# Kernel tuning notes

Measured on AMD Instinct MI355X. Metric: run time of the kernel, lower is better.

## Reference

```python
import jax, jax.numpy as jnp
import numpy as np

B, N = 4, 8192


def _nn_idx(a, b):
    # For each point in a [B,Na,3], index of nearest point in b [B,Nb,3].
    # ||a-b||^2 = ||a||^2 - 2 a.b + ||b||^2 ; ||a||^2 is constant per row -> drop it.
    d = jnp.sum(b * b, axis=-1)[:, None, :] - 2.0 * jnp.einsum('bnd,bmd->bnm', a, b)
    return jnp.argmin(d, axis=-1)  # [B, Na]


def _thickness(white, pial):
    # Mirrors compute_thickness_vector: white = inner, pial = outer.
    bix = jnp.arange(white.shape[0])[:, None]
    i1 = _nn_idx(white, pial)            # NN in pial for each white point
    inner_th = pial[bix, i1] - white     # [B, Nw, 3]
    i2 = _nn_idx(pial, white)            # NN in white for each pial point
    outer_th = pial - white[bix, i2]     # [B, Np, 3]
    return inner_th, outer_th


def _msn(a, b):
    # MeanSquaredNormLoss with w=None: mean over all points of sum((a-b)^2, -1)
    return jnp.mean(jnp.sum((a - b) ** 2, axis=-1))


def _sym(a, b, i_a, i_b):
    # SymmetricMeanSquaredNormLoss.forward (batch_size > 1 path, no weights)
    bix = jnp.arange(a.shape[0])[:, None]
    return 0.5 * (_msn(a, b[bix, i_a]) + _msn(a[bix, i_b], b))


def setup_inputs() -> dict:
    key = jax.random.key(0)
    ks = jax.random.split(key, 8)
    return {
        'pred_white': jax.random.normal(ks[0], (B, N, 3), jnp.float32),
        'pred_pial': jax.random.normal(ks[1], (B, N, 3), jnp.float32),
        'true_white': jax.random.normal(ks[2], (B, N, 3), jnp.float32),
        'true_pial': jax.random.normal(ks[3], (B, N, 3), jnp.float32),
        'i_pred_white': jax.random.randint(ks[4], (B, N), 0, N, jnp.int32),
        'i_true_white': jax.random.randint(ks[5], (B, N), 0, N, jnp.int32),
        'i_pred_pial': jax.random.randint(ks[6], (B, N), 0, N, jnp.int32),
        'i_true_pial': jax.random.randint(ks[7], (B, N), 0, N, jnp.int32),
    }


def reference(pred_white, pred_pial, true_white, true_pial,
              i_pred_white, i_true_white, i_pred_pial, i_true_pial):
    yp_inner, yp_outer = _thickness(pred_white, pred_pial)
    yt_inner, yt_outer = _thickness(true_white, true_pial)
    return (0.5 * _sym(yp_inner, yt_inner, i_pred_white, i_true_white)
            + 0.5 * _sym(yp_outer, yt_outer, i_pred_pial, i_true_pial))
```

## Files before the change

kernel.cpp:

```cpp
#include <hip/hip_runtime.h>
#include <math.h>

#define BATCH 4
#define NPTS 8192
#define BN (BATCH * NPTS)
#define NZB 16
#define QK 8
#define QBLK (256 * QK)
#define SUBT 64


__device__ __forceinline__ void pick_ab(int z, const float* pw, const float* pp,
                                        const float* tw, const float* tp,
                                        const float** qa, const float** cb) {
  if (z == 0)      { *qa = pw; *cb = pp; }
  else if (z == 1) { *qa = pp; *cb = pw; }
  else if (z == 2) { *qa = tw; *cb = tp; }
  else             { *qa = tp; *cb = tw; }
}

template <int SPL>
__global__ __launch_bounds__(256, 4) void nn_partial_kernel(
    const float* __restrict__ pw, const float* __restrict__ pp,
    const float* __restrict__ tw, const float* __restrict__ tp,
    float* __restrict__ part_d, unsigned char* __restrict__ part_t) {
  constexpr int SLICE = NPTS / SPL;
  constexpr int NSUB = SLICE / SUBT;
  __shared__ float4 sh[SLICE];

  const int zb = blockIdx.z;
  const int z = zb >> 2;
  const int b = zb & 3;
  const float* qa;
  const float* cb;
  pick_ab(z, pw, pp, tw, tp, &qa, &cb);

  const int tid = threadIdx.x;
  const int cslice = blockIdx.y * SLICE;
  const float* cbb = cb + (size_t)b * NPTS * 3;

  for (int m = tid; m < SLICE; m += 256) {
    const float* c = cbb + (size_t)(cslice + m) * 3;
    const float bx = c[0], by = c[1], bz = c[2];
    sh[m] = make_float4(bx, by, bz, fmaf(bx, bx, fmaf(by, by, bz * bz)));
  }
  __syncthreads();

  const int qbase = blockIdx.x * QBLK;
  float qx[QK], qy[QK], qz[QK], dmin[QK];
  int tile[QK];
  #pragma unroll
  for (int k = 0; k < QK; ++k) {
    const int n = qbase + tid + k * 256;
    const float* q = qa + ((size_t)b * NPTS + n) * 3;
    qx[k] = -2.0f * q[0];
    qy[k] = -2.0f * q[1];
    qz[k] = -2.0f * q[2];
    dmin[k] = INFINITY;
    tile[k] = 0;
  }

  for (int sub = 0; sub < NSUB; ++sub) {
    float pre[QK];
    #pragma unroll
    for (int k = 0; k < QK; ++k) pre[k] = dmin[k];

    const int cb0 = sub * SUBT;
    #pragma unroll 2
    for (int p = 0; p < SUBT / 2; ++p) {
      const float4 c0 = sh[cb0 + 2 * p];
      const float4 c1 = sh[cb0 + 2 * p + 1];
      float t0[QK], t1[QK];
      #pragma unroll
      for (int k = 0; k < QK; ++k)
        t0[k] = fmaf(qx[k], c0.x, fmaf(qy[k], c0.y, fmaf(qz[k], c0.z, c0.w)));
      #pragma unroll
      for (int k = 0; k < QK; ++k)
        t1[k] = fmaf(qx[k], c1.x, fmaf(qy[k], c1.y, fmaf(qz[k], c1.z, c1.w)));
      #pragma unroll
      for (int k = 0; k < QK; ++k)
        dmin[k] = fminf(fminf(t0[k], t1[k]), dmin[k]);
    }
    const int g = blockIdx.y * NSUB + sub;
    #pragma unroll
    for (int k = 0; k < QK; ++k)
      tile[k] = (dmin[k] < pre[k]) ? g : tile[k];
  }

  #pragma unroll
  for (int k = 0; k < QK; ++k) {
    const int n = qbase + tid + k * 256;
    const size_t o = (size_t)blockIdx.y * (NZB * NPTS) + (size_t)zb * NPTS + n;
    part_d[o] = dmin[k];
    part_t[o] = (unsigned char)tile[k];
  }
}

template <int SPL>
__global__ __launch_bounds__(1024) void nn_merge_rescan_kernel(
    const float* __restrict__ pw, const float* __restrict__ pp,
    const float* __restrict__ tw, const float* __restrict__ tp,
    const float* __restrict__ part_d, const unsigned char* __restrict__ part_t,
    int* __restrict__ idx_all, double* __restrict__ acc,
    unsigned int* __restrict__ ticket) {
  __shared__ float md[16][64];
  __shared__ int mg[16][64];
  __shared__ float sdq[64];
  __shared__ int sgq[64];

  if (blockIdx.x == 0 && threadIdx.x == 0) { *acc = 0.0; *ticket = 0u; }

  const int tid = threadIdx.x;
  const int wv = tid >> 6;
  const int lane = tid & 63;
  const int qid0 = blockIdx.x * 64;

  {
    float bd = INFINITY;
    int bg = 0x7fffffff;
    for (int s = wv; s < SPL; s += 16) {
      const size_t o = (size_t)s * (NZB * NPTS) + qid0 + lane;
      const float d = part_d[o];
      const int g = part_t[o];
      if (d < bd || (d == bd && g < bg)) { bd = d; bg = g; }
    }
    md[wv][lane] = bd;
    mg[wv][lane] = bg;
  }
  __syncthreads();
  if (wv == 0) {
    float bd = md[0][lane];
    int bg = mg[0][lane];
    #pragma unroll
    for (int v = 1; v < 16; ++v) {
      const float d = md[v][lane];
      const int g = mg[v][lane];
      if (d < bd || (d == bd && g < bg)) { bd = d; bg = g; }
    }
    sdq[lane] = bd;
    sgq[lane] = bg;
  }
  __syncthreads();

  const int zb = qid0 >> 13;
  const int z = zb >> 2;
  const int b = zb & 3;
  const float* qa;
  const float* cb;
  pick_ab(z, pw, pp, tw, tp, &qa, &cb);
  const float* qb0 = qa + (size_t)b * NPTS * 3;
  const float* cbb = cb + (size_t)b * NPTS * 3;
  const int n0 = qid0 & (NPTS - 1);

  #pragma unroll
  for (int j = 0; j < 4; ++j) {
    const int lq = wv * 4 + j;
    const float best_d = sdq[lq];
    const int best_g = sgq[lq];
    const float* q = qb0 + (size_t)(n0 + lq) * 3;
    const float qx = -2.0f * q[0];
    const float qy = -2.0f * q[1];
    const float qz = -2.0f * q[2];
    const int m = best_g * SUBT + lane;
    const float* c = cbb + (size_t)m * 3;
    const float bx = c[0], by = c[1], bz = c[2];
    const float b2 = fmaf(bx, bx, fmaf(by, by, bz * bz));
    const float dd = fmaf(qx, bx, fmaf(qy, by, fmaf(qz, bz, b2)));
    const unsigned long long hit = __ballot(dd == best_d);
    if (lane == 0)
      idx_all[qid0 + lq] = best_g * SUBT + (__ffsll((long long)hit) - 1);
  }
}

__device__ __forceinline__ float3 ld3(const float* __restrict__ p, int i) {
  const float* q = p + (size_t)i * 3;
  return make_float3(q[0], q[1], q[2]);
}

__device__ __forceinline__ float diff_nrm2(float3 a1, float3 a2, float3 b1, float3 b2) {
  const float x = (a1.x - a2.x) - (b1.x - b2.x);
  const float y = (a1.y - a2.y) - (b1.y - b2.y);
  const float z = (a1.z - a2.z) - (b1.z - b2.z);
  return fmaf(x, x, fmaf(y, y, z * z));
}

__global__ __launch_bounds__(256) void loss_final_kernel(
    const float* __restrict__ pw, const float* __restrict__ pp,
    const float* __restrict__ tw, const float* __restrict__ tp,
    const int* __restrict__ ipw, const int* __restrict__ itw,
    const int* __restrict__ ipp, const int* __restrict__ itp,
    const int* __restrict__ idx_all, double* __restrict__ acc,
    unsigned int* __restrict__ ticket, float* __restrict__ out) {
  __shared__ double sd[4];

  const int gid = blockIdx.x * 256 + threadIdx.x;
  const int term = blockIdx.y;
  const int b = gid >> 13;
  const int n = gid & (NPTS - 1);
  const int base = b * NPTS;

  const float* PW = pw + (size_t)base * 3;
  const float* PP = pp + (size_t)base * 3;
  const float* TW = tw + (size_t)base * 3;
  const float* TP = tp + (size_t)base * 3;
  const int* I1P = idx_all + (0 * BATCH + b) * NPTS;
  const int* I2P = idx_all + (1 * BATCH + b) * NPTS;
  const int* I1T = idx_all + (2 * BATCH + b) * NPTS;
  const int* I2T = idx_all + (3 * BATCH + b) * NPTS;

  float sv;
  if (term == 0) {
    const int j = ipw[base + n];
    sv = diff_nrm2(ld3(PP, I1P[n]), ld3(PW, n), ld3(TP, I1T[j]), ld3(TW, j));
  } else if (term == 1) {
    const int k = itw[base + n];
    sv = diff_nrm2(ld3(PP, I1P[k]), ld3(PW, k), ld3(TP, I1T[n]), ld3(TW, n));
  } else if (term == 2) {
    const int j = ipp[base + n];
    sv = diff_nrm2(ld3(PP, n), ld3(PW, I2P[n]), ld3(TP, j), ld3(TW, I2T[j]));
  } else {
    const int k = itp[base + n];
    sv = diff_nrm2(ld3(PP, k), ld3(PW, I2P[k]), ld3(TP, n), ld3(TW, I2T[n]));
  }

  double ds = (double)sv;
  #pragma unroll
  for (int o = 32; o > 0; o >>= 1) ds += __shfl_down(ds, o, 64);
  if ((threadIdx.x & 63) == 0) sd[threadIdx.x >> 6] = ds;
  __syncthreads();

  if (threadIdx.x == 0) {
    const double bsum = sd[0] + sd[1] + sd[2] + sd[3];
    const double old = atomicAdd(acc, bsum);
    const unsigned int inc = 1u + (unsigned int)(((unsigned long long)
                             __double_as_longlong(old)) & 0ull);
    const unsigned int total = gridDim.x * gridDim.y;
    const unsigned int t = atomicAdd(ticket, inc);
    if (t == total - 1u) {
      const double fin = atomicAdd(acc, 0.0);
      out[0] = (float)(0.25 * fin / (double)BN);
    }
  }
}

template <int SPL>
static void run_pipeline(const float* pw, const float* pp, const float* tw,
                         const float* tp, const int* ipw, const int* itw,
                         const int* ipp, const int* itp, char* ws, float* out,
                         hipStream_t stream) {
  double* acc = (double*)ws;
  unsigned int* ticket = (unsigned int*)(ws + 8);
  int* idx_all = (int*)(ws + 64);
  float* part_d = (float*)(ws + 64 + (size_t)NZB * NPTS * 4);
  unsigned char* part_t =
      (unsigned char*)(ws + 64 + (size_t)NZB * NPTS * 4 +
                       (size_t)SPL * NZB * NPTS * 4);

  dim3 grid_nn(NPTS / QBLK, SPL, NZB);
  nn_partial_kernel<SPL><<<grid_nn, 256, 0, stream>>>(pw, pp, tw, tp, part_d,
                                                      part_t);
  nn_merge_rescan_kernel<SPL><<<(NZB * NPTS) / 64, 1024, 0, stream>>>(
      pw, pp, tw, tp, part_d, part_t, idx_all, acc, ticket);

  dim3 grid_loss(BN / 256, 4);
  loss_final_kernel<<<grid_loss, 256, 0, stream>>>(
      pw, pp, tw, tp, ipw, itw, ipp, itp, idx_all, acc, ticket, out);
}

extern "C" void kernel_launch(void* const* d_in, const int* in_sizes, int n_in,
                              void* d_out, int out_size, void* d_ws, size_t ws_size,
                              hipStream_t stream) {
  const float* pw = (const float*)d_in[0];
  const float* pp = (const float*)d_in[1];
  const float* tw = (const float*)d_in[2];
  const float* tp = (const float*)d_in[3];
  const int* ipw = (const int*)d_in[4];
  const int* itw = (const int*)d_in[5];
  const int* ipp = (const int*)d_in[6];
  const int* itp = (const int*)d_in[7];
  char* ws = (char*)d_ws;
  float* out = (float*)d_out;

  const size_t base_need = 64 + (size_t)NZB * NPTS * 4;
  const size_t per_spl = (size_t)NZB * NPTS * 5;
  if (ws_size >= base_need + 32 * per_spl) {
    run_pipeline<32>(pw, pp, tw, tp, ipw, itw, ipp, itp, ws, out, stream);
  } else if (ws_size >= base_need + 16 * per_spl) {
    run_pipeline<16>(pw, pp, tw, tp, ipw, itw, ipp, itp, ws, out, stream);
  } else {
    run_pipeline<8>(pw, pp, tw, tp, ipw, itw, ipp, itp, ws, out, stream);
  }
}
```

Baseline: 180.0 us.

## Merge split-wise nearest-neighbour partials with packed 64-bit atomicMin instead of merge pass

Result: faster. 175.9 us (-2.3%).

```diff
diff --git a/kernel.cpp b/kernel.cpp
--- a/kernel.cpp
+++ b/kernel.cpp
@@ -8,6 +8,7 @@
 #define QK 8
 #define QBLK (256 * QK)
 #define SUBT 64
+#define SPL 32
 
 
 __device__ __forceinline__ void pick_ab(int z, const float* pw, const float* pp,
@@ -19,11 +20,18 @@
   else             { *qa = tp; *cb = tw; }
 }
 
-template <int SPL>
+__global__ __launch_bounds__(256) void init_kernel(
+    unsigned long long* __restrict__ packed, double* __restrict__ acc,
+    unsigned int* __restrict__ ticket) {
+  const int gid = blockIdx.x * 256 + threadIdx.x;
+  packed[gid] = 0xFFFFFFFFFFFFFFFFULL;
+  if (gid == 0) { *acc = 0.0; *ticket = 0u; }
+}
+
 __global__ __launch_bounds__(256, 4) void nn_partial_kernel(
     const float* __restrict__ pw, const float* __restrict__ pp,
     const float* __restrict__ tw, const float* __restrict__ tp,
-    float* __restrict__ part_d, unsigned char* __restrict__ part_t) {
+    unsigned long long* __restrict__ packed) {
   constexpr int SLICE = NPTS / SPL;
   constexpr int NSUB = SLICE / SUBT;
   __shared__ float4 sh[SLICE];
@@ -90,73 +98,45 @@
   #pragma unroll
   for (int k = 0; k < QK; ++k) {
     const int n = qbase + tid + k * 256;
-    const size_t o = (size_t)blockIdx.y * (NZB * NPTS) + (size_t)zb * NPTS + n;
-    part_d[o] = dmin[k];
-    part_t[o] = (unsigned char)tile[k];
-  }
-}
-
-template <int SPL>
-__global__ __launch_bounds__(1024) void nn_merge_rescan_kernel(
+    const unsigned int fb = __float_as_uint(dmin[k]);
+    const unsigned int key =
+        fb ^ ((fb & 0x80000000u) ? 0xFFFFFFFFu : 0x80000000u);
+    const unsigned long long pk =
+        ((unsigned long long)key << 32) | (unsigned int)tile[k];
+    atomicMin(&packed[(size_t)zb * NPTS + n], pk);
+  }
+}
+
+__global__ __launch_bounds__(256) void nn_rescan_kernel(
     const float* __restrict__ pw, const float* __restrict__ pp,
     const float* __restrict__ tw, const float* __restrict__ tp,
-    const float* __restrict__ part_d, const unsigned char* __restrict__ part_t,
-    int* __restrict__ idx_all, double* __restrict__ acc,
-    unsigned int* __restrict__ ticket) {
-  __shared__ float md[16][64];
-  __shared__ int mg[16][64];
-  __shared__ float sdq[64];
-  __shared__ int sgq[64];
-
-  if (blockIdx.x == 0 && threadIdx.x == 0) { *acc = 0.0; *ticket = 0u; }
-
+    const unsigned long long* __restrict__ packed,
+    int* __restrict__ idx_all) {
   const int tid = threadIdx.x;
   const int wv = tid >> 6;
   const int lane = tid & 63;
-  const int qid0 = blockIdx.x * 64;
-
-  {
-    float bd = INFINITY;
-    int bg = 0x7fffffff;
-    for (int s = wv; s < SPL; s += 16) {
-      const size_t o = (size_t)s * (NZB * NPTS) + qid0 + lane;
-      const float d = part_d[o];
-      const int g = part_t[o];
-      if (d < bd || (d == bd && g < bg)) { bd = d; bg = g; }
-    }
-    md[wv][lane] = bd;
-    mg[wv][lane] = bg;
-  }
-  __syncthreads();
-  if (wv == 0) {
-    float bd = md[0][lane];
-    int bg = mg[0][lane];
-    #pragma unroll
-    for (int v = 1; v < 16; ++v) {
-      const float d = md[v][lane];
-      const int g = mg[v][lane];
-      if (d < bd || (d == bd && g < bg)) { bd = d; bg = g; }
-    }
-    sdq[lane] = bd;
-    sgq[lane] = bg;
-  }
-  __syncthreads();
+  const int qid0 = blockIdx.x * 32;
 
   const int zb = qid0 >> 13;
   const int z = zb >> 2;
   const int b = zb & 3;
   const float* qa;
-  const float* cb;
-  pick_ab(z, pw, pp, tw, tp, &qa, &cb);
+  const float* cbp;
+  pick_ab(z, pw, pp, tw, tp, &qa, &cbp);
   const float* qb0 = qa + (size_t)b * NPTS * 3;
-  const float* cbb = cb + (size_t)b * NPTS * 3;
+  const float* cbb = cbp + (size_t)b * NPTS * 3;
   const int n0 = qid0 & (NPTS - 1);
 
   #pragma unroll
-  for (int j = 0; j < 4; ++j) {
-    const int lq = wv * 4 + j;
-    const float best_d = sdq[lq];
-    const int best_g = sgq[lq];
+  for (int j = 0; j < 8; ++j) {
+    const int lq = wv * 8 + j;
+    const unsigned long long pk = packed[qid0 + lq];
+    const int best_g = (int)(pk & 0xFFFFFFFFULL);
+    const unsigned int key = (unsigned int)(pk >> 32);
+    const unsigned int fb =
+        (key & 0x80000000u) ? (key ^ 0x80000000u) : ~key;
+    const float best_d = __uint_as_float(fb);
+
     const float* q = qb0 + (size_t)(n0 + lq) * 3;
     const float qx = -2.0f * q[0];
     const float qy = -2.0f * q[1];
@@ -243,30 +223,6 @@
   }
 }
 
-template <int SPL>
-static void run_pipeline(const float* pw, const float* pp, const float* tw,
-                         const float* tp, const int* ipw, const int* itw,
-                         const int* ipp, const int* itp, char* ws, float* out,
-                         hipStream_t stream) {
-  double* acc = (double*)ws;
-  unsigned int* ticket = (unsigned int*)(ws + 8);
-  int* idx_all = (int*)(ws + 64);
-  float* part_d = (float*)(ws + 64 + (size_t)NZB * NPTS * 4);
-  unsigned char* part_t =
-      (unsigned char*)(ws + 64 + (size_t)NZB * NPTS * 4 +
-                       (size_t)SPL * NZB * NPTS * 4);
-
-  dim3 grid_nn(NPTS / QBLK, SPL, NZB);
-  nn_partial_kernel<SPL><<<grid_nn, 256, 0, stream>>>(pw, pp, tw, tp, part_d,
-                                                      part_t);
-  nn_merge_rescan_kernel<SPL><<<(NZB * NPTS) / 64, 1024, 0, stream>>>(
-      pw, pp, tw, tp, part_d, part_t, idx_all, acc, ticket);
-
-  dim3 grid_loss(BN / 256, 4);
-  loss_final_kernel<<<grid_loss, 256, 0, stream>>>(
-      pw, pp, tw, tp, ipw, itw, ipp, itp, idx_all, acc, ticket, out);
-}
-
 extern "C" void kernel_launch(void* const* d_in, const int* in_sizes, int n_in,
                               void* d_out, int out_size, void* d_ws, size_t ws_size,
                               hipStream_t stream) {
@@ -281,13 +237,21 @@
   char* ws = (char*)d_ws;
   float* out = (float*)d_out;
 
-  const size_t base_need = 64 + (size_t)NZB * NPTS * 4;
-  const size_t per_spl = (size_t)NZB * NPTS * 5;
-  if (ws_size >= base_need + 32 * per_spl) {
-    run_pipeline<32>(pw, pp, tw, tp, ipw, itw, ipp, itp, ws, out, stream);
-  } else if (ws_size >= base_need + 16 * per_spl) {
-    run_pipeline<16>(pw, pp, tw, tp, ipw, itw, ipp, itp, ws, out, stream);
-  } else {
-    run_pipeline<8>(pw, pp, tw, tp, ipw, itw, ipp, itp, ws, out, stream);
-  }
-}
+  double* acc = (double*)ws;
+  unsigned int* ticket = (unsigned int*)(ws + 8);
+  int* idx_all = (int*)(ws + 64);
+  unsigned long long* packed =
+      (unsigned long long*)(ws + 64 + (size_t)NZB * NPTS * 4);
+
+  init_kernel<<<(NZB * NPTS) / 256, 256, 0, stream>>>(packed, acc, ticket);
+
+  dim3 grid_nn(NPTS / QBLK, SPL, NZB);
+  nn_partial_kernel<<<grid_nn, 256, 0, stream>>>(pw, pp, tw, tp, packed);
+
+  nn_rescan_kernel<<<(NZB * NPTS) / 32, 256, 0, stream>>>(
+      pw, pp, tw, tp, packed, idx_all);
+
+  dim3 grid_loss(BN / 256, 4);
+  loss_final_kernel<<<grid_loss, 256, 0, stream>>>(
+      pw, pp, tw, tp, ipw, itw, ipp, itp, idx_all, acc, ticket, out);
+}
```
